# Optimization experiments

Measured on AMD Instinct MI355X. Metric: run time of the kernel, lower is better.

The kernel has to match this reference:

```python
import jax, jax.numpy as jnp
import numpy as np

B, H, S, D = 2, 12, 3456, 32
FEATS_PER_T = 216
WINDOW_LEN = 8
ACT_SIZE = 16
IMG_FEAT_SIZE = 196
DECODER_ONLY = False


def eye_mask(seq_len, feats_per_t, window_len, act_size, img_feat_size, decoder_only=False):
    """Boolean [S, S] mask replicating get_eye_block_mask's memory_mask."""
    idx = jnp.arange(seq_len)
    q_t = (idx // feats_per_t)[:, None]          # [S,1]
    kv_t = (idx // feats_per_t)[None, :]         # [1,S]
    q_m = (idx % feats_per_t)[:, None]
    kv_m = (idx % feats_per_t)[None, :]
    proprio_idx_mod = 2 + 1 + 1
    img_start = feats_per_t - img_feat_size
    joint_start = img_start - act_size

    causal = (q_t >= kv_t) & (q_t - kv_t < window_len)
    is_q_img = q_m >= img_start
    is_kv_img = kv_m >= img_start
    is_q_joint = (q_m >= joint_start) & (q_m < img_start)
    is_kv_joint = (kv_m >= joint_start) & (kv_m < img_start)
    is_kv_proprio = kv_m == proprio_idx_mod

    img_to_img = ~(is_q_img & is_kv_img)
    same_t = q_t == kv_t
    joint_past_joint = ~(is_q_joint & is_kv_joint & ~same_t)
    proprio_past = ~(is_kv_proprio & (kv_t < q_t))
    past_image = ~(is_kv_img & (kv_t < q_t))
    m = causal & img_to_img & joint_past_joint & proprio_past & past_image
    if decoder_only:
        m = m & ~(is_q_img & ~is_kv_img)
    return m


def setup_inputs() -> dict:
    key = jax.random.key(0)
    kq, kk, kv = jax.random.split(key, 3)
    return {
        "q": jax.random.normal(kq, (B, H, S, D), dtype=jnp.float32),
        "k": jax.random.normal(kk, (B, H, S, D), dtype=jnp.float32),
        "v": jax.random.normal(kv, (B, H, S, D), dtype=jnp.float32),
        "feats_per_t": FEATS_PER_T,
        "window_len": WINDOW_LEN,
        "act_size": ACT_SIZE,
        "img_feat_size": IMG_FEAT_SIZE,
    }


def reference(q, k, v, feats_per_t, window_len, act_size, img_feat_size):
    seq_len = q.shape[2]
    mask = eye_mask(seq_len, feats_per_t, window_len, act_size,
                    img_feat_size, DECODER_ONLY)  # [S,S]
    scale = 1.0 / jnp.sqrt(jnp.array(q.shape[-1], q.dtype))
    scores = jnp.einsum("bhqd,bhkd->bhqk", q, k) * scale
    neg = jnp.asarray(jnp.finfo(scores.dtype).min, scores.dtype)
    scores = jnp.where(mask[None, None], scores, neg)
    attn = jax.nn.softmax(scores, axis=-1)
    return jnp.einsum("bhqk,bhkd->bhqd", attn, v)
```

## Files before the change

kernel.cpp:

```cpp
#include <hip/hip_runtime.h>

#define SEQ   3456
#define DH    32
#define FPT   216
#define NT    16
#define IMG0  20
#define SCALE2 0.2550707067f

#define KPAD   40
#define VPAD   168
#define IPAD   232
#define PPITCH 40

typedef __attribute__((ext_vector_type(8))) short bf16x8;
typedef __attribute__((ext_vector_type(4))) float f32x4;

#define MFMA16(a,b,c) __builtin_amdgcn_mfma_f32_16x16x32_bf16(a,b,c,0,0,0)

__device__ __forceinline__ unsigned short bfh(float f) {
    unsigned u = __float_as_uint(f);
    u += 0x7FFFu + ((u >> 16) & 1u);
    return (unsigned short)(u >> 16);
}
__device__ __forceinline__ float bff(unsigned short h) {
    return __uint_as_float((unsigned)h << 16);
}
__device__ __forceinline__ void split8(const float* f, bf16x8& hi, bf16x8& lo) {
    #pragma unroll
    for (int j = 0; j < 8; ++j) {
        unsigned short h = bfh(f[j]);
        hi[j] = (short)h;
        lo[j] = (short)bfh(f[j] - bff(h));
    }
}

__constant__ unsigned MN_TAB[5] = {0xFEFFFFFFu, 0xFFFFEFFFu, 0xFFEFFFFEu,
                                   0xEFFFFEFFu, 0xFFFEFFFFu};
__constant__ unsigned MJ_TAB[5] = {0x00FFFFFFu, 0xF0000F00u, 0x000F0000u,
                                   0x0F0000F0u, 0x0000F000u};

__global__ __launch_bounds__(256)
void eye_attn_mfma6(const float* __restrict__ q, const float* __restrict__ k,
                    const float* __restrict__ v, float* __restrict__ out) {
    __shared__ __align__(16) unsigned short KsHi[160 * KPAD];
    __shared__ __align__(16) unsigned short VtHi[DH * VPAD];
    __shared__ __align__(16) unsigned short VtImg[DH * IPAD];
    __shared__ __align__(16) unsigned short Pu[4 * 16 * PPITCH];

    const int t = blockIdx.x, bh = blockIdx.y, half = blockIdx.z;
    const int tid = threadIdx.x;
    const size_t base = (size_t)bh * SEQ * DH;
    const int dmax = (t < 7) ? t : 7;
    const int nkeys = IMG0 * (dmax + 1);
    const int nkt = (nkeys + 31) >> 5;

    for (int i = tid; i < nkeys * 8; i += 256) {
        const int g = i >> 3, c = i & 7;
        const int d = g / IMG0, jj = g - d * IMG0;
        const size_t row = base + (size_t)((t - d) * FPT + jj) * DH + c * 4;
        const float4 kk = *(const float4*)(k + row);
        const float4 vv = *(const float4*)(v + row);
        const float kf[4] = {kk.x, kk.y, kk.z, kk.w};
        const float vf[4] = {vv.x, vv.y, vv.z, vv.w};
        ushort4 khi;
        unsigned short* ah = (unsigned short*)&khi;
        #pragma unroll
        for (int e = 0; e < 4; ++e) ah[e] = bfh(kf[e]);
        *(ushort4*)(KsHi + g * KPAD + c * 4) = khi;
        #pragma unroll
        for (int e = 0; e < 4; ++e)
            VtHi[(c * 4 + e) * VPAD + g] = bfh(vf[e]);
    }
    {
        const int rem = nkeys - (nkt - 1) * 32;
        if (rem < 32) {
            for (int i = tid; i < 1024; i += 256) {
                const int c = i & 31;
                if (c >= rem)
                    VtHi[(i >> 5) * VPAD + (nkt - 1) * 32 + c] = 0;
            }
        }
    }
    if (half == 0) {
        for (int i = tid; i < 1792; i += 256) {
            const int gi = i >> 3, c = i & 7;
            float4 vv = make_float4(0.f, 0.f, 0.f, 0.f);
            if (gi < 196) {
                const size_t row = base + (size_t)(t * FPT + IMG0 + gi) * DH + c * 4;
                vv = *(const float4*)(v + row);
            }
            const float vf[4] = {vv.x, vv.y, vv.z, vv.w};
            #pragma unroll
            for (int e = 0; e < 4; ++e)
                VtImg[(c * 4 + e) * IPAD + gi] = bfh(vf[e]);
        }
    }
    __syncthreads();

    const int wv = tid >> 6, lane = tid & 63;
    const int col = lane & 15, quad = lane >> 4;

    unsigned mNt[5], mJt[5];
    #pragma unroll
    for (int kt = 0; kt < 5; ++kt) {
        const int tr = nkeys - kt * 32;
        unsigned mn = MN_TAB[kt], mj = MJ_TAB[kt];
        if (tr <= 0) { mn = 0u; mj = 0u; }
        else if (tr < 32) { const unsigned lim = (1u << tr) - 1u; mn &= lim; mj &= lim; }
        mNt[kt] = mn; mJt[kt] = mj;
    }

    bf16x8 bones;
    #pragma unroll
    for (int j = 0; j < 8; ++j) bones[j] = (short)(col == 0 ? 0x3F80 : 0);

    unsigned short* myP = Pu + wv * 16 * PPITCH;

    int mt[2]; int mcnt; bool do_img = false;
    if (half == 0) {
        if (wv == 0)      { mt[0] = 0; mcnt = 1; do_img = true; }
        else if (wv == 1) { mt[0] = 1; mcnt = 1; do_img = true; }
        else if (wv == 2) { mt[0] = 2; mt[1] = 3; mcnt = 2; }
        else              { mt[0] = 4; mt[1] = 5; mcnt = 2; }
    } else {
        mt[0] = 6 + 2 * wv; mt[1] = 7 + 2 * wv; mcnt = 2;
    }

    for (int mi = 0; mi < mcnt; ++mi) {
        const int mb = mt[mi] * 16;
        bf16x8 qhi, qlo;
        {
            const int qc = min(mb + col, FPT - 1);
            const float* qp = q + base + (size_t)(t * FPT + qc) * DH + quad * 8;
            float qf[8];
            const float4 a0 = *(const float4*)qp;
            const float4 a1 = *(const float4*)(qp + 4);
            qf[0]=a0.x*SCALE2; qf[1]=a0.y*SCALE2; qf[2]=a0.z*SCALE2; qf[3]=a0.w*SCALE2;
            qf[4]=a1.x*SCALE2; qf[5]=a1.y*SCALE2; qf[6]=a1.z*SCALE2; qf[7]=a1.w*SCALE2;
            split8(qf, qhi, qlo);
        }
        f32x4 oacc0 = {0.f,0.f,0.f,0.f}, oacc1 = {0.f,0.f,0.f,0.f};
        f32x4 lacc = {0.f,0.f,0.f,0.f};

        for (int kt = 0; kt < nkt; ++kt) {
            f32x4 s[2];
            #pragma unroll
            for (int h = 0; h < 2; ++h) {
                const int key = kt * 32 + h * 16 + col;
                const bf16x8 khi = *(const bf16x8*)(KsHi + key * KPAD + quad * 8);
                f32x4 acc = {0.f,0.f,0.f,0.f};
                acc = MFMA16(qhi, khi, acc);
                acc = MFMA16(qlo, khi, acc);
                s[h] = acc;
            }
            #pragma unroll
            for (int r = 0; r < 4; ++r) {
                const int qm = mb + quad * 4 + r;
                const bool isj = (qm >= 4) && (qm < IMG0);
                const unsigned m = (qm < FPT) ? (isj ? mJt[kt] : mNt[kt]) : 0u;
                #pragma unroll
                for (int h = 0; h < 2; ++h) {
                    const float e = ((m >> (h * 16 + col)) & 1u)
                                    ? exp2f(s[h][r]) : 0.f;
                    myP[(quad * 4 + r) * PPITCH + h * 16 + col] = bfh(e);
                }
            }
            const bf16x8 phi = *(const bf16x8*)(myP + col * PPITCH + quad * 8);
            #pragma unroll
            for (int h = 0; h < 2; ++h) {
                const int dim = h * 16 + col;
                const bf16x8 vhi = *(const bf16x8*)(VtHi + dim * VPAD + kt * 32 + quad * 8);
                f32x4& oa = h ? oacc1 : oacc0;
                oa = MFMA16(phi, vhi, oa);
            }
            lacc = MFMA16(phi, bones, lacc);
        }

        if (mi == 0 && do_img) {
            for (int kt2 = 0; kt2 < 7; ++kt2) {
                f32x4 s[2];
                #pragma unroll
                for (int h = 0; h < 2; ++h) {
                    const int keyc = min(IMG0 + kt2 * 32 + h * 16 + col, FPT - 1);
                    const float* kp = k + base + (size_t)(t * FPT + keyc) * DH + quad * 8;
                    float kf[8];
                    const float4 a0 = *(const float4*)kp;
                    const float4 a1 = *(const float4*)(kp + 4);
                    kf[0]=a0.x; kf[1]=a0.y; kf[2]=a0.z; kf[3]=a0.w;
                    kf[4]=a1.x; kf[5]=a1.y; kf[6]=a1.z; kf[7]=a1.w;
                    bf16x8 khi;
                    #pragma unroll
                    for (int j = 0; j < 8; ++j) khi[j] = (short)bfh(kf[j]);
                    f32x4 acc = {0.f,0.f,0.f,0.f};
                    acc = MFMA16(qhi, khi, acc);
                    acc = MFMA16(qlo, khi, acc);
                    s[h] = acc;
                }
                #pragma unroll
                for (int h = 0; h < 2; ++h) {
                    const int key = IMG0 + kt2 * 32 + h * 16 + col;
                    #pragma unroll
                    for (int r = 0; r < 4; ++r) {
                        const int qm = mb + quad * 4 + r;
                        const bool vis = (key < FPT) && (qm < IMG0);
                        const float e = vis ? exp2f(s[h][r]) : 0.f;
                        myP[(quad * 4 + r) * PPITCH + h * 16 + col] = bfh(e);
                    }
                }
                const bf16x8 phi = *(const bf16x8*)(myP + col * PPITCH + quad * 8);
                #pragma unroll
                for (int h = 0; h < 2; ++h) {
                    const int dim = h * 16 + col;
                    const bf16x8 vhi = *(const bf16x8*)(VtImg + dim * IPAD + kt2 * 32 + quad * 8);
                    f32x4& oa = h ? oacc1 : oacc0;
                    oa = MFMA16(phi, vhi, oa);
                }
                lacc = MFMA16(phi, bones, lacc);
            }
        }

        #pragma unroll
        for (int r = 0; r < 4; ++r) {
            const float lr = __shfl(lacc[r], lane & 48);
            const float inv = 1.f / lr;
            const int qm = mb + quad * 4 + r;
            if (qm < FPT) {
                float* op = out + base + (size_t)(t * FPT + qm) * DH;
                op[col]      = oacc0[r] * inv;
                op[16 + col] = oacc1[r] * inv;
            }
        }
    }
}

extern "C" void kernel_launch(void* const* d_in, const int* in_sizes, int n_in,
                              void* d_out, int out_size, void* d_ws, size_t ws_size,
                              hipStream_t stream) {
    const float* q = (const float*)d_in[0];
    const float* k = (const float*)d_in[1];
    const float* v = (const float*)d_in[2];
    float* out = (float*)d_out;
    const int BH = in_sizes[0] / (SEQ * DH);
    dim3 grid(NT, BH, 2);
    eye_attn_mfma6<<<grid, 256, 0, stream>>>(q, k, v, out);
}
```

Baseline: 99.14 us.

## Interleave two query tiles per wave and fuse image loop with sparse loop

Each wave now processes its two 16-row query tiles together in one key loop, sharing K/V LDS reads and issuing independent MFMA chains for more instruction-level parallelism. Image-key waves fuse the sparse-key loop and the image-key loop into one pass with separate accumulators, summed at the end. Q loads are hoisted before the K/V staging loop so their global latency overlaps the staging. Launch bounds request 3 blocks per CU and the P scratch buffer doubles, which raises register and LDS pressure.

```diff
diff --git a/kernel.cpp b/kernel.cpp
--- a/kernel.cpp
+++ b/kernel.cpp
@@ -39,13 +39,13 @@
 __constant__ unsigned MJ_TAB[5] = {0x00FFFFFFu, 0xF0000F00u, 0x000F0000u,
                                    0x0F0000F0u, 0x0000F000u};
 
-__global__ __launch_bounds__(256)
-void eye_attn_mfma6(const float* __restrict__ q, const float* __restrict__ k,
+__global__ __launch_bounds__(256, 3)
+void eye_attn_mfma7(const float* __restrict__ q, const float* __restrict__ k,
                     const float* __restrict__ v, float* __restrict__ out) {
     __shared__ __align__(16) unsigned short KsHi[160 * KPAD];
     __shared__ __align__(16) unsigned short VtHi[DH * VPAD];
     __shared__ __align__(16) unsigned short VtImg[DH * IPAD];
-    __shared__ __align__(16) unsigned short Pu[4 * 16 * PPITCH];
+    __shared__ __align__(16) unsigned short Pu[8 * 16 * PPITCH];
 
     const int t = blockIdx.x, bh = blockIdx.y, half = blockIdx.z;
     const int tid = threadIdx.x;
@@ -53,6 +53,28 @@
     const int dmax = (t < 7) ? t : 7;
     const int nkeys = IMG0 * (dmax + 1);
     const int nkt = (nkeys + 31) >> 5;
+
+    const int wv = tid >> 6, lane = tid & 63;
+    const int col = lane & 15, quad = lane >> 4;
+
+    int tA, tB = 0; bool do_img = false;
+    if (half == 0) {
+        if (wv < 2) { tA = wv; do_img = true; }
+        else        { tA = (wv - 2) * 2 + 2; tB = tA + 1; }
+    } else {
+        tA = 6 + 2 * wv; tB = tA + 1;
+    }
+    const int mbA = tA * 16, mbB = tB * 16;
+
+    const float* qpA = q + base + (size_t)(t * FPT + min(mbA + col, FPT - 1)) * DH + quad * 8;
+    const float4 qA0 = ((const float4*)qpA)[0];
+    const float4 qA1 = ((const float4*)qpA)[1];
+    float4 qB0 = qA0, qB1 = qA1;
+    if (!do_img) {
+        const float* qpB = q + base + (size_t)(t * FPT + min(mbB + col, FPT - 1)) * DH + quad * 8;
+        qB0 = ((const float4*)qpB)[0];
+        qB1 = ((const float4*)qpB)[1];
+    }
 
     for (int i = tid; i < nkeys * 8; i += 256) {
         const int g = i >> 3, c = i & 7;
@@ -97,9 +119,6 @@
     }
     __syncthreads();
 
-    const int wv = tid >> 6, lane = tid & 63;
-    const int col = lane & 15, quad = lane >> 4;
-
     unsigned mNt[5], mJt[5];
     #pragma unroll
     for (int kt = 0; kt < 5; ++kt) {
@@ -114,120 +133,183 @@
     #pragma unroll
     for (int j = 0; j < 8; ++j) bones[j] = (short)(col == 0 ? 0x3F80 : 0);
 
-    unsigned short* myP = Pu + wv * 16 * PPITCH;
-
-    int mt[2]; int mcnt; bool do_img = false;
-    if (half == 0) {
-        if (wv == 0)      { mt[0] = 0; mcnt = 1; do_img = true; }
-        else if (wv == 1) { mt[0] = 1; mcnt = 1; do_img = true; }
-        else if (wv == 2) { mt[0] = 2; mt[1] = 3; mcnt = 2; }
-        else              { mt[0] = 4; mt[1] = 5; mcnt = 2; }
-    } else {
-        mt[0] = 6 + 2 * wv; mt[1] = 7 + 2 * wv; mcnt = 2;
-    }
-
-    for (int mi = 0; mi < mcnt; ++mi) {
-        const int mb = mt[mi] * 16;
-        bf16x8 qhi, qlo;
-        {
-            const int qc = min(mb + col, FPT - 1);
-            const float* qp = q + base + (size_t)(t * FPT + qc) * DH + quad * 8;
-            float qf[8];
-            const float4 a0 = *(const float4*)qp;
-            const float4 a1 = *(const float4*)(qp + 4);
-            qf[0]=a0.x*SCALE2; qf[1]=a0.y*SCALE2; qf[2]=a0.z*SCALE2; qf[3]=a0.w*SCALE2;
-            qf[4]=a1.x*SCALE2; qf[5]=a1.y*SCALE2; qf[6]=a1.z*SCALE2; qf[7]=a1.w*SCALE2;
-            split8(qf, qhi, qlo);
-        }
-        f32x4 oacc0 = {0.f,0.f,0.f,0.f}, oacc1 = {0.f,0.f,0.f,0.f};
-        f32x4 lacc = {0.f,0.f,0.f,0.f};
-
+    unsigned short* PA = Pu + (wv * 2 + 0) * 16 * PPITCH;
+    unsigned short* PB = Pu + (wv * 2 + 1) * 16 * PPITCH;
+
+    bf16x8 qAhi, qAlo, qBhi, qBlo;
+    {
+        float qf[8];
+        qf[0]=qA0.x*SCALE2; qf[1]=qA0.y*SCALE2; qf[2]=qA0.z*SCALE2; qf[3]=qA0.w*SCALE2;
+        qf[4]=qA1.x*SCALE2; qf[5]=qA1.y*SCALE2; qf[6]=qA1.z*SCALE2; qf[7]=qA1.w*SCALE2;
+        split8(qf, qAhi, qAlo);
+    }
+    if (!do_img) {
+        float qf[8];
+        qf[0]=qB0.x*SCALE2; qf[1]=qB0.y*SCALE2; qf[2]=qB0.z*SCALE2; qf[3]=qB0.w*SCALE2;
+        qf[4]=qB1.x*SCALE2; qf[5]=qB1.y*SCALE2; qf[6]=qB1.z*SCALE2; qf[7]=qB1.w*SCALE2;
+        split8(qf, qBhi, qBlo);
+    }
+
+    if (!do_img) {
+        f32x4 aO0={0.f,0.f,0.f,0.f}, aO1={0.f,0.f,0.f,0.f}, aL={0.f,0.f,0.f,0.f};
+        f32x4 bO0={0.f,0.f,0.f,0.f}, bO1={0.f,0.f,0.f,0.f}, bL={0.f,0.f,0.f,0.f};
         for (int kt = 0; kt < nkt; ++kt) {
-            f32x4 s[2];
+            f32x4 sA[2], sB[2];
             #pragma unroll
             for (int h = 0; h < 2; ++h) {
                 const int key = kt * 32 + h * 16 + col;
                 const bf16x8 khi = *(const bf16x8*)(KsHi + key * KPAD + quad * 8);
-                f32x4 acc = {0.f,0.f,0.f,0.f};
-                acc = MFMA16(qhi, khi, acc);
-                acc = MFMA16(qlo, khi, acc);
-                s[h] = acc;
+                f32x4 x = {0.f,0.f,0.f,0.f};
+                x = MFMA16(qAhi, khi, x);
+                x = MFMA16(qAlo, khi, x);
+                sA[h] = x;
+                f32x4 y = {0.f,0.f,0.f,0.f};
+                y = MFMA16(qBhi, khi, y);
+                y = MFMA16(qBlo, khi, y);
+                sB[h] = y;
             }
             #pragma unroll
             for (int r = 0; r < 4; ++r) {
-                const int qm = mb + quad * 4 + r;
-                const bool isj = (qm >= 4) && (qm < IMG0);
-                const unsigned m = (qm < FPT) ? (isj ? mJt[kt] : mNt[kt]) : 0u;
+                const int qmA = mbA + quad * 4 + r;
+                const int qmB = mbB + quad * 4 + r;
+                const bool jA = (qmA >= 4) && (qmA < IMG0);
+                const bool jB = (qmB >= 4) && (qmB < IMG0);
+                const unsigned mA = (qmA < FPT) ? (jA ? mJt[kt] : mNt[kt]) : 0u;
+                const unsigned mB = (qmB < FPT) ? (jB ? mJt[kt] : mNt[kt]) : 0u;
                 #pragma unroll
                 for (int h = 0; h < 2; ++h) {
-                    const float e = ((m >> (h * 16 + col)) & 1u)
-                                    ? exp2f(s[h][r]) : 0.f;
-                    myP[(quad * 4 + r) * PPITCH + h * 16 + col] = bfh(e);
-                }
-            }
-            const bf16x8 phi = *(const bf16x8*)(myP + col * PPITCH + quad * 8);
+                    const int bit = h * 16 + col;
+                    const float eA = ((mA >> bit) & 1u) ? exp2f(sA[h][r]) : 0.f;
+                    const float eB = ((mB >> bit) & 1u) ? exp2f(sB[h][r]) : 0.f;
+                    PA[(quad * 4 + r) * PPITCH + bit] = bfh(eA);
+                    PB[(quad * 4 + r) * PPITCH + bit] = bfh(eB);
+                }
+            }
+            const bf16x8 pA = *(const bf16x8*)(PA + col * PPITCH + quad * 8);
+            const bf16x8 pB = *(const bf16x8*)(PB + col * PPITCH + quad * 8);
             #pragma unroll
             for (int h = 0; h < 2; ++h) {
                 const int dim = h * 16 + col;
                 const bf16x8 vhi = *(const bf16x8*)(VtHi + dim * VPAD + kt * 32 + quad * 8);
-                f32x4& oa = h ? oacc1 : oacc0;
-                oa = MFMA16(phi, vhi, oa);
-            }
-            lacc = MFMA16(phi, bones, lacc);
-        }
-
-        if (mi == 0 && do_img) {
-            for (int kt2 = 0; kt2 < 7; ++kt2) {
-                f32x4 s[2];
+                if (h == 0) { aO0 = MFMA16(pA, vhi, aO0); bO0 = MFMA16(pB, vhi, bO0); }
+                else        { aO1 = MFMA16(pA, vhi, aO1); bO1 = MFMA16(pB, vhi, bO1); }
+            }
+            aL = MFMA16(pA, bones, aL);
+            bL = MFMA16(pB, bones, bL);
+        }
+        #pragma unroll
+        for (int r = 0; r < 4; ++r) {
+            const float lr = __shfl(aL[r], lane & 48);
+            const float inv = 1.f / lr;
+            const int qm = mbA + quad * 4 + r;
+            if (qm < FPT) {
+                float* op = out + base + (size_t)(t * FPT + qm) * DH;
+                op[col] = aO0[r] * inv; op[16 + col] = aO1[r] * inv;
+            }
+        }
+        #pragma unroll
+        for (int r = 0; r < 4; ++r) {
+            const float lr = __shfl(bL[r], lane & 48);
+            const float inv = 1.f / lr;
+            const int qm = mbB + quad * 4 + r;
+            if (qm < FPT) {
+                float* op = out + base + (size_t)(t * FPT + qm) * DH;
+                op[col] = bO0[r] * inv; op[16 + col] = bO1[r] * inv;
+            }
+        }
+    } else {
+        f32x4 sO0={0.f,0.f,0.f,0.f}, sO1={0.f,0.f,0.f,0.f}, sL={0.f,0.f,0.f,0.f};
+        f32x4 iO0={0.f,0.f,0.f,0.f}, iO1={0.f,0.f,0.f,0.f}, iL={0.f,0.f,0.f,0.f};
+        for (int it = 0; it < 7; ++it) {
+            float4 ik0[2], ik1[2];
+            #pragma unroll
+            for (int h = 0; h < 2; ++h) {
+                const int keyc = min(IMG0 + it * 32 + h * 16 + col, FPT - 1);
+                const float* kp = k + base + (size_t)(t * FPT + keyc) * DH + quad * 8;
+                ik0[h] = ((const float4*)kp)[0];
+                ik1[h] = ((const float4*)kp)[1];
+            }
+            const bool doS = it < nkt;
+            f32x4 sS[2], sI[2];
+            if (doS) {
                 #pragma unroll
                 for (int h = 0; h < 2; ++h) {
-                    const int keyc = min(IMG0 + kt2 * 32 + h * 16 + col, FPT - 1);
-                    const float* kp = k + base + (size_t)(t * FPT + keyc) * DH + quad * 8;
-                    float kf[8];
-                    const float4 a0 = *(const float4*)kp;
-                    const float4 a1 = *(const float4*)(kp + 4);
-                    kf[0]=a0.x; kf[1]=a0.y; kf[2]=a0.z; kf[3]=a0.w;
-                    kf[4]=a1.x; kf[5]=a1.y; kf[6]=a1.z; kf[7]=a1.w;
-                    bf16x8 khi;
+                    const int key = it * 32 + h * 16 + col;
+                    const bf16x8 khi = *(const bf16x8*)(KsHi + key * KPAD + quad * 8);
+                    f32x4 x = {0.f,0.f,0.f,0.f};
+                    x = MFMA16(qAhi, khi, x);
+                    x = MFMA16(qAlo, khi, x);
+                    sS[h] = x;
+                }
+            }
+            #pragma unroll
+            for (int h = 0; h < 2; ++h) {
+                float kf[8];
+                kf[0]=ik0[h].x; kf[1]=ik0[h].y; kf[2]=ik0[h].z; kf[3]=ik0[h].w;
+                kf[4]=ik1[h].x; kf[5]=ik1[h].y; kf[6]=ik1[h].z; kf[7]=ik1[h].w;
+                bf16x8 khi;
+                #pragma unroll
+                for (int j = 0; j < 8; ++j) khi[j] = (short)bfh(kf[j]);
+                f32x4 x = {0.f,0.f,0.f,0.f};
+                x = MFMA16(qAhi, khi, x);
+                x = MFMA16(qAlo, khi, x);
+                sI[h] = x;
+            }
+            if (doS) {
+                #pragma unroll
+                for (int r = 0; r < 4; ++r) {
+                    const int qm = mbA + quad * 4 + r;
+                    const bool isj = (qm >= 4) && (qm < IMG0);
+                    const unsigned m = isj ? mJt[it] : mNt[it];
                     #pragma unroll
-                    for (int j = 0; j < 8; ++j) khi[j] = (short)bfh(kf[j]);
-                    f32x4 acc = {0.f,0.f,0.f,0.f};
-                    acc = MFMA16(qhi, khi, acc);
-                    acc = MFMA16(qlo, khi, acc);
-                    s[h] = acc;
-                }
-                #pragma unroll
-                for (int h = 0; h < 2; ++h) {
-                    const int key = IMG0 + kt2 * 32 + h * 16 + col;
-                    #pragma unroll
-                    for (int r = 0; r < 4; ++r) {
-                        const int qm = mb + quad * 4 + r;
-                        const bool vis = (key < FPT) && (qm < IMG0);
-                        const float e = vis ? exp2f(s[h][r]) : 0.f;
-                        myP[(quad * 4 + r) * PPITCH + h * 16 + col] = bfh(e);
+                    for (int h = 0; h < 2; ++h) {
+                        const int bit = h * 16 + col;
+                        const float e = ((m >> bit) & 1u) ? exp2f(sS[h][r]) : 0.f;
+                        PA[(quad * 4 + r) * PPITCH + bit] = bfh(e);
                     }
                 }
-                const bf16x8 phi = *(const bf16x8*)(myP + col * PPITCH + quad * 8);
+            }
+            #pragma unroll
+            for (int h = 0; h < 2; ++h) {
+                const int key = IMG0 + it * 32 + h * 16 + col;
+                #pragma unroll
+                for (int r = 0; r < 4; ++r) {
+                    const int qm = mbA + quad * 4 + r;
+                    const bool vis = (key < FPT) && (qm < IMG0);
+                    const float e = vis ? exp2f(sI[h][r]) : 0.f;
+                    PB[(quad * 4 + r) * PPITCH + h * 16 + col] = bfh(e);
+                }
+            }
+            if (doS) {
+                const bf16x8 pA = *(const bf16x8*)(PA + col * PPITCH + quad * 8);
                 #pragma unroll
                 for (int h = 0; h < 2; ++h) {
                     const int dim = h * 16 + col;
-                    const bf16x8 vhi = *(const bf16x8*)(VtImg + dim * IPAD + kt2 * 32 + quad * 8);
-                    f32x4& oa = h ? oacc1 : oacc0;
-                    oa = MFMA16(phi, vhi, oa);
-                }
-                lacc = MFMA16(phi, bones, lacc);
-            }
-        }
-
+                    const bf16x8 vhi = *(const bf16x8*)(VtHi + dim * VPAD + it * 32 + quad * 8);
+                    if (h == 0) sO0 = MFMA16(pA, vhi, sO0);
+                    else        sO1 = MFMA16(pA, vhi, sO1);
+                }
+                sL = MFMA16(pA, bones, sL);
+            }
+            const bf16x8 pB = *(const bf16x8*)(PB + col * PPITCH + quad * 8);
+            #pragma unroll
+            for (int h = 0; h < 2; ++h) {
+                const int dim = h * 16 + col;
+                const bf16x8 vhi = *(const bf16x8*)(VtImg + dim * IPAD + it * 32 + quad * 8);
+                if (h == 0) iO0 = MFMA16(pB, vhi, iO0);
+                else        iO1 = MFMA16(pB, vhi, iO1);
+            }
+            iL = MFMA16(pB, bones, iL);
+        }
+        const f32x4 o0 = sO0 + iO0, o1 = sO1 + iO1, lt = sL + iL;
         #pragma unroll
         for (int r = 0; r < 4; ++r) {
-            const float lr = __shfl(lacc[r], lane & 48);
+            const float lr = __shfl(lt[r], lane & 48);
             const float inv = 1.f / lr;
-            const int qm = mb + quad * 4 + r;
+            const int qm = mbA + quad * 4 + r;
             if (qm < FPT) {
                 float* op = out + base + (size_t)(t * FPT + qm) * DH;
-                op[col]      = oacc0[r] * inv;
-                op[16 + col] = oacc1[r] * inv;
+                op[col] = o0[r] * inv; op[16 + col] = o1[r] * inv;
             }
         }
     }
@@ -242,5 +324,5 @@
     float* out = (float*)d_out;
     const int BH = in_sizes[0] / (SEQ * DH);
     dim3 grid(NT, BH, 2);
-    eye_attn_mfma6<<<grid, 256, 0, stream>>>(q, k, v, out);
-}
+    eye_attn_mfma7<<<grid, 256, 0, stream>>>(q, k, v, out);
+}
```

Measured after the change: 102.7 us. +3.6%, slower.
